# Performance work log

Measured on AMD Instinct MI355X. Metric: run time of the kernel, lower is better.

## Reference

```python
import jax, jax.numpy as jnp
import numpy as np

MASK_FILL = -1e9
LN_EPS = 1e-5


def setup_inputs() -> dict:
    key = jax.random.key(0)
    ks = jax.random.split(key, 8)
    b, n, d = 4, 4096, 768
    k, ds = 64, 32
    x = jax.random.normal(ks[0], (b, n, d), dtype=jnp.float32)
    encoded_descriptions = jax.random.normal(ks[1], (k, ds, d), dtype=jnp.float32)
    description_attention_mask = jax.random.randint(ks[2], (k, ds), 0, 2).astype(jnp.int32)
    attention_masks = jax.random.randint(ks[3], (b, n), 0, 2).astype(jnp.int32)
    std = 0.03
    Wk = std * jax.random.normal(ks[4], (d, d), dtype=jnp.float32)
    Wv = std * jax.random.normal(ks[5], (d, d), dtype=jnp.float32)
    Wo = std * jax.random.normal(ks[6], (1, d), dtype=jnp.float32)
    bo = jnp.zeros((1,), dtype=jnp.float32)
    ln_gamma = jnp.ones((d,), dtype=jnp.float32)
    ln_beta = jnp.zeros((d,), dtype=jnp.float32)
    return {
        "x": x,
        "encoded_descriptions": encoded_descriptions,
        "description_attention_mask": description_attention_mask,
        "attention_masks": attention_masks,
        "Wk": Wk, "Wv": Wv, "Wo": Wo, "bo": bo,
        "ln_gamma": ln_gamma, "ln_beta": ln_beta,
    }


def reference(x, encoded_descriptions, description_attention_mask, attention_masks,
              Wk, Wv, Wo, bo, ln_gamma, ln_beta):
    # x: [b, n, d]; encoded_descriptions: [k, ds, d]
    d = x.shape[-1]
    scale = 1.0 / jnp.sqrt(jnp.float32(d))

    k_note = jnp.einsum('bni,oi->bno', x, Wk)  # nn.Linear: x @ W.T
    v_note = jnp.einsum('bni,oi->bno', x, Wv)

    # att: [b, k, ds, n]  (torch computes kdbn then permutes to bkdn)
    att = jnp.einsum('kdi,bni->bkdn', encoded_descriptions, k_note) * scale

    desc_mask = description_attention_mask.astype(bool)          # [k, ds]
    note_mask = attention_masks.astype(bool)                     # [b, n]
    combined = desc_mask[None, :, :, None] & note_mask[:, None, None, :]  # [b,k,ds,n]

    att = jnp.where(combined, att, MASK_FILL)
    attention = jax.nn.softmax(att, axis=-1)                     # [b,k,ds,n]

    context = jnp.einsum('bkdn,bni->bkdi', attention, v_note)    # [b,k,ds,d]

    desc_importance = attention.sum(axis=-1)                     # [b,k,ds]
    desc_importance = jnp.where(desc_mask[None, :, :], desc_importance, MASK_FILL)
    desc_weights = jax.nn.softmax(desc_importance, axis=-1)      # [b,k,ds]

    pooled = (context * desc_weights[..., None]).sum(axis=2)     # [b,k,d]

    mu = pooled.mean(axis=-1, keepdims=True)
    var = pooled.var(axis=-1, keepdims=True)
    y = (pooled - mu) * jax.lax.rsqrt(var + LN_EPS) * ln_gamma + ln_beta

    out = jnp.einsum('bkd,od->bko', y, Wo) + bo                  # [b,k,1]
    return out[..., 0]                                           # [b,k]
```

## Files before the change

kernel.cpp:

```cpp
#include <hip/hip_runtime.h>
#include <hip/hip_bf16.h>
#include <hip/hip_fp16.h>

typedef _Float16 half8 __attribute__((ext_vector_type(8)));
typedef _Float16 half4 __attribute__((ext_vector_type(4)));
typedef _Float16 half2v __attribute__((ext_vector_type(2)));
typedef float f32x4 __attribute__((ext_vector_type(4)));

#define LN_EPS 1e-5f
#define MASK_FILL -1e9f

__device__ __forceinline__ void async16(void* lds, const void* g) {
  __builtin_amdgcn_global_load_lds(
      (__attribute__((address_space(1))) void*)(g),
      (__attribute__((address_space(3))) void*)(lds), 16, 0, 0);
}

__global__ __launch_bounds__(256) void cast_f32_f16_kernel(
    const float* __restrict__ in, _Float16* __restrict__ out, int n4) {
  int i = blockIdx.x * 256 + threadIdx.x;
  if (i < n4) {
    float4 v = ((const float4*)in)[i];
    half4 h = { (_Float16)v.x, (_Float16)v.y, (_Float16)v.z, (_Float16)v.w };
    ((half4*)out)[i] = h;
  }
}

__global__ __launch_bounds__(256) void transpose_f32_to_f16_kernel(
    const float* __restrict__ in, _Float16* __restrict__ out, int R, int C) {
  __shared__ float tile[32][33];
  int bc = blockIdx.x * 32, br = blockIdx.y * 32;
  int lc = threadIdx.x & 31;
  int lr0 = threadIdx.x >> 5;
  for (int i = lr0; i < 32; i += 8)
    tile[i][lc] = in[(size_t)(br + i) * C + bc + lc];
  __syncthreads();
  for (int i = lr0; i < 32; i += 8)
    out[(size_t)(bc + i) * R + br + lc] = (_Float16)tile[lc][i];
}

__global__ __launch_bounds__(256) void prep_kernel(
    const int* __restrict__ dmask, int* __restrict__ rowmap,
    float* __restrict__ row_w, int* __restrict__ start, int* __restrict__ keepM) {
  __shared__ int lsum[256];
  __shared__ int nvs[64];
  const int tid = threadIdx.x;
  int flags[8];
  int cnt = 0;
#pragma unroll
  for (int u = 0; u < 8; u++) {
    flags[u] = dmask[tid * 8 + u] != 0;
    cnt += flags[u];
  }
  if (tid < 64) {
    int c = 0;
    for (int u = 0; u < 32; u++) c += (dmask[tid * 32 + u] != 0);
    nvs[tid] = c;
  }
  lsum[tid] = cnt;
  __syncthreads();
  for (int ofs = 1; ofs < 256; ofs <<= 1) {
    int t = (tid >= ofs) ? lsum[tid - ofs] : 0;
    __syncthreads();
    lsum[tid] += t;
    __syncthreads();
  }
  int excl = lsum[tid] - cnt;
  int pos = excl;
#pragma unroll
  for (int u = 0; u < 8; u++) {
    if (flags[u]) {
      int row = tid * 8 + u;
      rowmap[pos] = row;
      row_w[pos] = 1.0f / (float)nvs[row >> 5];
      pos++;
    }
  }
  if ((tid & 3) == 0) start[tid >> 2] = excl;
  if (tid == 255) {
    start[64] = lsum[255];
    *keepM = lsum[255];
  }
}

__global__ __launch_bounds__(256) void gather_cast_kernel(
    const float* __restrict__ src, const int* __restrict__ rowmap,
    const int* __restrict__ keepM, _Float16* __restrict__ dst) {
  const int r = blockIdx.x;
  const int t = threadIdx.x;
  const int k = *keepM;
  _Float16* d = dst + (size_t)r * 768;
  if (r < k) {
    const float* s = src + (size_t)rowmap[r] * 768;
    for (int i = t; i < 768; i += 256) d[i] = (_Float16)s[i];
  } else {
    int* di = (int*)d;
    for (int i = t; i < 384; i += 256) di[i] = 0;
  }
}

template<bool OUT_F32, bool XCD>
__global__ __launch_bounds__(256) void gemm_f16_kernel(
    const _Float16* __restrict__ A, const _Float16* __restrict__ Bt,
    void* __restrict__ C, int M, int N, int K, float alpha,
    size_t strideBt, size_t strideC, const int* __restrict__ keepRows) {
  int bx = blockIdx.x, by = blockIdx.y, bz = blockIdx.z;
  if (XCD) {
    const int gx = gridDim.x, gy = gridDim.y;
    const int total = gx * gy * gridDim.z;
    const int L = bx + gx * (by + gy * bz);
    const int orig = (L & 7) * (total >> 3) + (L >> 3);
    bx = orig % gx;
    const int rest = orig / gx;
    by = rest % gy;
    bz = rest / gy;
  }
  const int bm = bx * 128, bn = by * 128;
  if (keepRows && bm >= *keepRows) return;
  __shared__ _Float16 As[128 * 64];
  __shared__ _Float16 Bs[128 * 64];
  const int tid = threadIdx.x;
  const size_t z = bz;
  const int wave = tid >> 6, lane = tid & 63;
  const int wr = (wave >> 1) * 64, wc = (wave & 1) * 64;
  const int fr = lane & 15, xr = lane & 7;
  f32x4 acc[4][4] = {};
  const int srow = wave * 32 + (lane >> 3);
  const int scol = (((lane & 7) ^ (lane >> 3))) * 8;
  const _Float16* ga = A + (size_t)(bm + srow) * K + scol;
  const _Float16* gb = Bt + z * strideBt + (size_t)(bn + srow) * K + scol;
  _Float16* lA = &As[(wave * 32) * 64];
  _Float16* lB = &Bs[(wave * 32) * 64];
  for (int k0 = 0; k0 < K; k0 += 64) {
    __syncthreads();
#pragma unroll
    for (int i = 0; i < 4; i++) {
      async16(lA + i * 8 * 64, ga + (size_t)(8 * i) * K + k0);
      async16(lB + i * 8 * 64, gb + (size_t)(8 * i) * K + k0);
    }
    __syncthreads();
#pragma unroll
    for (int k2 = 0; k2 < 2; k2++) {
      const int sb = k2 * 4 + (lane >> 4);
      const int so = (sb ^ xr) * 8;
      half8 af[4], bf[4];
#pragma unroll
      for (int i = 0; i < 4; i++)
        af[i] = *(const half8*)&As[(wr + i * 16 + fr) * 64 + so];
#pragma unroll
      for (int j = 0; j < 4; j++)
        bf[j] = *(const half8*)&Bs[(wc + j * 16 + fr) * 64 + so];
#pragma unroll
      for (int i = 0; i < 4; i++)
#pragma unroll
        for (int j = 0; j < 4; j++)
          acc[i][j] = __builtin_amdgcn_mfma_f32_16x16x32_f16(af[i], bf[j], acc[i][j], 0, 0, 0);
    }
  }
  const int rg = (lane >> 4) * 4;
#pragma unroll
  for (int i = 0; i < 4; i++) {
#pragma unroll
    for (int j = 0; j < 4; j++) {
      int col = bn + wc + j * 16 + fr;
#pragma unroll
      for (int r = 0; r < 4; r++) {
        int row = bm + wr + i * 16 + rg + r;
        float v = acc[i][j][r] * alpha;
        if (OUT_F32)
          ((float*)C)[z * strideC + (size_t)row * N + col] = v;
        else
          ((_Float16*)C)[z * strideC + (size_t)row * N + col] = (_Float16)v;
      }
    }
  }
}

__device__ __forceinline__ float block_reduce(float v, bool do_max, float* wbuf, int tid) {
#pragma unroll
  for (int m = 32; m; m >>= 1) {
    float o = __shfl_xor(v, m);
    v = do_max ? fmaxf(v, o) : (v + o);
  }
  if ((tid & 63) == 0) wbuf[tid >> 6] = v;
  __syncthreads();
  float r = do_max ? fmaxf(fmaxf(wbuf[0], wbuf[1]), fmaxf(wbuf[2], wbuf[3]))
                   : (wbuf[0] + wbuf[1] + wbuf[2] + wbuf[3]);
  __syncthreads();
  return r;
}

__global__ __launch_bounds__(256) void row_stats_kernel(
    const _Float16* __restrict__ S, const float* __restrict__ row_w,
    const int* __restrict__ keepM, const int* __restrict__ amask,
    float4* __restrict__ stats_c) {
  const int r = blockIdx.x;
  if (r >= *keepM) return;
  __shared__ float wbuf[4];
  const int b = blockIdx.z;
  const int tid = threadIdx.x;
  const float w = row_w[r];
  const _Float16* sp = S + ((size_t)b * 2048 + r) * 4096;
  const int* am = amask + (size_t)b * 4096;
  float a[16];
#pragma unroll
  for (int h = 0; h < 2; h++) {
    half8 v = *(const half8*)(sp + h * 2048 + tid * 8);
    int4 m0 = *(const int4*)(am + h * 2048 + tid * 8);
    int4 m1 = *(const int4*)(am + h * 2048 + tid * 8 + 4);
    int mm[8] = {m0.x, m0.y, m0.z, m0.w, m1.x, m1.y, m1.z, m1.w};
#pragma unroll
    for (int u = 0; u < 8; u++)
      a[h * 8 + u] = (mm[u] != 0) ? (float)v[u] : MASK_FILL;
  }
  float mx = a[0];
#pragma unroll
  for (int c = 1; c < 16; c++) mx = fmaxf(mx, a[c]);
  mx = block_reduce(mx, true, wbuf, tid);
  float ls = 0.f;
#pragma unroll
  for (int c = 0; c < 16; c++) ls += expf(a[c] - mx);
  float denom = block_reduce(ls, false, wbuf, tid);
  if (tid == 0)
    stats_c[(size_t)b * 2048 + r] = make_float4(mx, w / denom, 0.f, 0.f);
}

__global__ __launch_bounds__(256) void combine_kernel(
    const _Float16* __restrict__ S, const float4* __restrict__ stats_c,
    const int* __restrict__ start, const int* __restrict__ amask,
    float* __restrict__ ca) {
  const int kd = blockIdx.x;
  const int b = blockIdx.z;
  const int n0 = blockIdx.y * 512 + threadIdx.x * 2;
  const int i0 = start[kd], i1 = start[kd + 1];
  float acc0, acc1;
  if (i0 == i1) {
    acc0 = acc1 = 1.0f / 4096.0f;
  } else {
    const int* am = amask + (size_t)b * 4096;
    const bool nm0 = am[n0] != 0, nm1 = am[n0 + 1] != 0;
    acc0 = 0.f;
    acc1 = 0.f;
    for (int i = i0; i < i1; i++) {
      float4 s4 = stats_c[(size_t)b * 2048 + i];
      half2v v = *(const half2v*)(S + ((size_t)b * 2048 + i) * 4096 + n0);
      float a0 = nm0 ? (float)v[0] : MASK_FILL;
      float a1 = nm1 ? (float)v[1] : MASK_FILL;
      acc0 += s4.y * expf(a0 - s4.x);
      acc1 += s4.y * expf(a1 - s4.x);
    }
  }
  float2 r = {acc0, acc1};
  *(float2*)&ca[((size_t)b * 64 + kd) * 4096 + n0] = r;
}

__global__ __launch_bounds__(256) void t_partial_kernel(
    const float* __restrict__ ca,
    const _Float16* __restrict__ xh,
    float* __restrict__ t_part) {
  __shared__ float cas[64][68];
  __shared__ float xs[64][132];
  const int jt = blockIdx.x;
  const int nc = blockIdx.y;
  const int b = blockIdx.z;
  const int tid = threadIdx.x;
  const int tm = tid >> 4, tj = tid & 15;
  const int r = tid >> 2;
  const int cg = (tid & 3) * 16;
  const int cc = (tid & 3) * 32;
  float acc[4][8] = {};
  for (int n0 = nc * 256; n0 < nc * 256 + 256; n0 += 64) {
    __syncthreads();
    const float* cap = ca + (size_t)(b * 64 + r) * 4096 + n0 + cg;
#pragma unroll
    for (int u = 0; u < 16; u += 4)
      *(float4*)&cas[r][cg + u] = *(const float4*)(cap + u);
    const _Float16* xp = xh + ((size_t)b * 4096 + n0 + r) * 768 + jt * 128 + cc;
#pragma unroll
    for (int u = 0; u < 32; u += 8) {
      half8 hv = *(const half8*)(xp + u);
#pragma unroll
      for (int q = 0; q < 8; q++) xs[r][cc + u + q] = (float)hv[q];
    }
    __syncthreads();
#pragma unroll 8
    for (int nn = 0; nn < 64; ++nn) {
      float cm[4], xj[8];
#pragma unroll
      for (int i = 0; i < 4; i++) cm[i] = cas[tm * 4 + i][nn];
#pragma unroll
      for (int j = 0; j < 8; j++) xj[j] = xs[nn][tj * 8 + j];
#pragma unroll
      for (int i = 0; i < 4; i++)
#pragma unroll
        for (int j = 0; j < 8; j++) acc[i][j] += cm[i] * xj[j];
    }
  }
#pragma unroll
  for (int i = 0; i < 4; i++)
#pragma unroll
    for (int j = 0; j < 8; j++)
      t_part[((size_t)nc * 256 + b * 64 + tm * 4 + i) * 768 + jt * 128 + tj * 8 + j] = acc[i][j];
}

__global__ __launch_bounds__(256) void t_reduce_kernel(
    const float* __restrict__ t_part, _Float16* __restrict__ th) {
  int i = blockIdx.x * 256 + threadIdx.x;
  float s = 0.f;
#pragma unroll
  for (int nc = 0; nc < 16; ++nc) s += t_part[(size_t)nc * 196608 + i];
  th[i] = (_Float16)s;
}

__global__ __launch_bounds__(256) void ln_out_kernel(
    const float* __restrict__ pooled, const float* __restrict__ Wo,
    const float* __restrict__ bo, const float* __restrict__ gamma,
    const float* __restrict__ beta, float* __restrict__ out) {
  __shared__ float wbuf[4];
  const int row = blockIdx.x, tid = threadIdx.x;
  float p[3];
#pragma unroll
  for (int u = 0; u < 3; u++) p[u] = pooled[(size_t)row * 768 + tid + u * 256];
  float s1 = p[0] + p[1] + p[2];
  float s2 = p[0] * p[0] + p[1] * p[1] + p[2] * p[2];
  s1 = block_reduce(s1, false, wbuf, tid);
  s2 = block_reduce(s2, false, wbuf, tid);
  float mean = s1 * (1.f / 768.f);
  float var = s2 * (1.f / 768.f) - mean * mean;
  float rstd = rsqrtf(var + LN_EPS);
  float accv = 0.f;
#pragma unroll
  for (int u = 0; u < 3; u++) {
    int i = tid + u * 256;
    float y = (p[u] - mean) * rstd * gamma[i] + beta[i];
    accv += y * Wo[i];
  }
  accv = block_reduce(accv, false, wbuf, tid);
  if (tid == 0) out[row] = accv + bo[0];
}

extern "C" void kernel_launch(void* const* d_in, const int* in_sizes, int n_in,
                              void* d_out, int out_size, void* d_ws, size_t ws_size,
                              hipStream_t stream) {
  const float* x = (const float*)d_in[0];
  const float* enc = (const float*)d_in[1];
  const int* dmask = (const int*)d_in[2];
  const int* amask = (const int*)d_in[3];
  const float* Wk = (const float*)d_in[4];
  const float* Wv = (const float*)d_in[5];
  const float* Wo = (const float*)d_in[6];
  const float* bo = (const float*)d_in[7];
  const float* gamma = (const float*)d_in[8];
  const float* beta = (const float*)d_in[9];
  float* out = (float*)d_out;

  char* ws = (char*)d_ws;
  size_t off = 0;
  auto alloc = [&](size_t bytes) -> char* {
    char* p = ws + off;
    off += (bytes + 255) & ~((size_t)255);
    return p;
  };
  _Float16* xh = (_Float16*)alloc((size_t)16384 * 768 * 2);
  _Float16* wkT = (_Float16*)alloc((size_t)768 * 768 * 2);
  _Float16* wvh = (_Float16*)alloc((size_t)768 * 768 * 2);
  _Float16* enc_c = (_Float16*)alloc((size_t)2048 * 768 * 2);
  _Float16* encK_c = (_Float16*)alloc((size_t)2048 * 768 * 2);
  float* ca = (float*)alloc((size_t)4 * 64 * 4096 * 4);
  float* t_part = (float*)alloc((size_t)16 * 256 * 768 * 4);
  _Float16* th = (_Float16*)alloc((size_t)256 * 768 * 2);
  float* pooled = (float*)alloc((size_t)256 * 768 * 4);
  float4* stats_c = (float4*)alloc((size_t)4 * 2048 * 16);
  int* rowmap = (int*)alloc(2048 * 4);
  float* row_w = (float*)alloc(2048 * 4);
  int* start = (int*)alloc(65 * 4);
  int* keepM = (int*)alloc(4);

  const size_t s_one = (size_t)2048 * 4096 * 2;
  const bool batched = (off + 4 * s_one) <= ws_size;
  _Float16* S = (_Float16*)alloc(batched ? 4 * s_one : s_one);

  const float scale = 0.036084391824351615f;

  prep_kernel<<<1, 256, 0, stream>>>(dmask, rowmap, row_w, start, keepM);
  cast_f32_f16_kernel<<<12288, 256, 0, stream>>>(x, xh, 16384 * 768 / 4);
  cast_f32_f16_kernel<<<576, 256, 0, stream>>>(Wv, wvh, 768 * 768 / 4);
  transpose_f32_to_f16_kernel<<<dim3(24, 24), 256, 0, stream>>>(Wk, wkT, 768, 768);
  gather_cast_kernel<<<2048, 256, 0, stream>>>(enc, rowmap, keepM, enc_c);

  gemm_f16_kernel<false, false><<<dim3(16, 6), 256, 0, stream>>>(
      enc_c, wkT, encK_c, 2048, 768, 768, 1.0f, 0, 0, keepM);

  if (batched) {
    gemm_f16_kernel<false, true><<<dim3(16, 32, 4), 256, 0, stream>>>(
        encK_c, xh, S, 2048, 4096, 768, scale,
        (size_t)4096 * 768, (size_t)2048 * 4096, keepM);
    row_stats_kernel<<<dim3(2048, 1, 4), 256, 0, stream>>>(
        S, row_w, keepM, amask, stats_c);
    combine_kernel<<<dim3(64, 8, 4), 256, 0, stream>>>(S, stats_c, start, amask, ca);
  } else {
    for (int b = 0; b < 4; b++) {
      gemm_f16_kernel<false, true><<<dim3(16, 32), 256, 0, stream>>>(
          encK_c, xh + (size_t)b * 4096 * 768, S, 2048, 4096, 768, scale, 0, 0, keepM);
      row_stats_kernel<<<dim3(2048, 1, 1), 256, 0, stream>>>(
          S, row_w, keepM, amask + (size_t)b * 4096, stats_c + (size_t)b * 2048);
      combine_kernel<<<dim3(64, 8, 1), 256, 0, stream>>>(
          S, stats_c + (size_t)b * 2048, start, amask + (size_t)b * 4096,
          ca + (size_t)b * 64 * 4096);
    }
  }

  t_partial_kernel<<<dim3(6, 16, 4), 256, 0, stream>>>(ca, xh, t_part);
  t_reduce_kernel<<<768, 256, 0, stream>>>(t_part, th);
  gemm_f16_kernel<true, false><<<dim3(2, 6), 256, 0, stream>>>(
      th, wvh, pooled, 256, 768, 768, 1.0f, 0, 0, nullptr);
  ln_out_kernel<<<256, 256, 0, stream>>>(pooled, Wo, bo, gamma, beta, out);
}
```

Baseline: 164.3 us.

## Double-buffer GEMM K-loop and fuse row softmax stats with combine

The f16 GEMM now uses a 32-wide K tile, two LDS buffers and async prefetch of the next tile while the current one feeds MFMA, with a new swizzle. The separate row-statistics and combine kernels are merged into one kernel per (description, batch) that loops over its rows, computing max, sum and weighted exponentials in registers. This avoids reading the score matrix twice and drops the stats buffer. The cost is a grid of only 256 blocks, each serially walking its rows with block-wide reductions, which cuts parallelism.

Result: slower. 180.4 us (+9.8%).

```diff
diff --git a/kernel.cpp b/kernel.cpp
--- a/kernel.cpp
+++ b/kernel.cpp
@@ -4,7 +4,6 @@
 
 typedef _Float16 half8 __attribute__((ext_vector_type(8)));
 typedef _Float16 half4 __attribute__((ext_vector_type(4)));
-typedef _Float16 half2v __attribute__((ext_vector_type(2)));
 typedef float f32x4 __attribute__((ext_vector_type(4)));
 
 #define LN_EPS 1e-5f
@@ -117,45 +116,47 @@
   }
   const int bm = bx * 128, bn = by * 128;
   if (keepRows && bm >= *keepRows) return;
-  __shared__ _Float16 As[128 * 64];
-  __shared__ _Float16 Bs[128 * 64];
+  __shared__ _Float16 As[2][128 * 32];
+  __shared__ _Float16 Bs[2][128 * 32];
   const int tid = threadIdx.x;
   const size_t z = bz;
   const int wave = tid >> 6, lane = tid & 63;
   const int wr = (wave >> 1) * 64, wc = (wave & 1) * 64;
-  const int fr = lane & 15, xr = lane & 7;
+  const int fr = lane & 15;
   f32x4 acc[4][4] = {};
-  const int srow = wave * 32 + (lane >> 3);
-  const int scol = (((lane & 7) ^ (lane >> 3))) * 8;
+  const int srow = wave * 32 + (lane >> 2);
+  const int scol = ((lane & 3) ^ ((lane >> 3) & 3)) * 8;
   const _Float16* ga = A + (size_t)(bm + srow) * K + scol;
   const _Float16* gb = Bt + z * strideBt + (size_t)(bn + srow) * K + scol;
-  _Float16* lA = &As[(wave * 32) * 64];
-  _Float16* lB = &Bs[(wave * 32) * 64];
-  for (int k0 = 0; k0 < K; k0 += 64) {
+  const int nt = K >> 5;
+  auto stage = [&](int buf, int k0) {
+    _Float16* la = &As[buf][(wave * 32) * 32];
+    _Float16* lb = &Bs[buf][(wave * 32) * 32];
+    async16(la, ga + k0);
+    async16(la + 16 * 32, ga + (size_t)16 * K + k0);
+    async16(lb, gb + k0);
+    async16(lb + 16 * 32, gb + (size_t)16 * K + k0);
+  };
+  const int sg = (((lane >> 4) ^ ((fr >> 1) & 3))) * 8;
+  stage(0, 0);
+  __syncthreads();
+  int cur = 0;
+  for (int t = 0; t < nt; ++t) {
+    if (t + 1 < nt) stage(cur ^ 1, (t + 1) * 32);
+    half8 af[4], bf[4];
+#pragma unroll
+    for (int i = 0; i < 4; i++)
+      af[i] = *(const half8*)&As[cur][(wr + i * 16 + fr) * 32 + sg];
+#pragma unroll
+    for (int j = 0; j < 4; j++)
+      bf[j] = *(const half8*)&Bs[cur][(wc + j * 16 + fr) * 32 + sg];
+#pragma unroll
+    for (int i = 0; i < 4; i++)
+#pragma unroll
+      for (int j = 0; j < 4; j++)
+        acc[i][j] = __builtin_amdgcn_mfma_f32_16x16x32_f16(af[i], bf[j], acc[i][j], 0, 0, 0);
     __syncthreads();
-#pragma unroll
-    for (int i = 0; i < 4; i++) {
-      async16(lA + i * 8 * 64, ga + (size_t)(8 * i) * K + k0);
-      async16(lB + i * 8 * 64, gb + (size_t)(8 * i) * K + k0);
-    }
-    __syncthreads();
-#pragma unroll
-    for (int k2 = 0; k2 < 2; k2++) {
-      const int sb = k2 * 4 + (lane >> 4);
-      const int so = (sb ^ xr) * 8;
-      half8 af[4], bf[4];
-#pragma unroll
-      for (int i = 0; i < 4; i++)
-        af[i] = *(const half8*)&As[(wr + i * 16 + fr) * 64 + so];
-#pragma unroll
-      for (int j = 0; j < 4; j++)
-        bf[j] = *(const half8*)&Bs[(wc + j * 16 + fr) * 64 + so];
-#pragma unroll
-      for (int i = 0; i < 4; i++)
-#pragma unroll
-        for (int j = 0; j < 4; j++)
-          acc[i][j] = __builtin_amdgcn_mfma_f32_16x16x32_f16(af[i], bf[j], acc[i][j], 0, 0, 0);
-    }
+    cur ^= 1;
   }
   const int rg = (lane >> 4) * 4;
 #pragma unroll
@@ -190,68 +191,69 @@
   return r;
 }
 
-__global__ __launch_bounds__(256) void row_stats_kernel(
+__global__ __launch_bounds__(256) void fused_softmax_kernel(
     const _Float16* __restrict__ S, const float* __restrict__ row_w,
-    const int* __restrict__ keepM, const int* __restrict__ amask,
-    float4* __restrict__ stats_c) {
-  const int r = blockIdx.x;
-  if (r >= *keepM) return;
+    const int* __restrict__ start, const int* __restrict__ amask,
+    float* __restrict__ ca) {
   __shared__ float wbuf[4];
+  const int kd = blockIdx.x;
   const int b = blockIdx.z;
   const int tid = threadIdx.x;
-  const float w = row_w[r];
-  const _Float16* sp = S + ((size_t)b * 2048 + r) * 4096;
-  const int* am = amask + (size_t)b * 4096;
-  float a[16];
-#pragma unroll
-  for (int h = 0; h < 2; h++) {
-    half8 v = *(const half8*)(sp + h * 2048 + tid * 8);
-    int4 m0 = *(const int4*)(am + h * 2048 + tid * 8);
-    int4 m1 = *(const int4*)(am + h * 2048 + tid * 8 + 4);
-    int mm[8] = {m0.x, m0.y, m0.z, m0.w, m1.x, m1.y, m1.z, m1.w};
-#pragma unroll
-    for (int u = 0; u < 8; u++)
-      a[h * 8 + u] = (mm[u] != 0) ? (float)v[u] : MASK_FILL;
-  }
-  float mx = a[0];
-#pragma unroll
-  for (int c = 1; c < 16; c++) mx = fmaxf(mx, a[c]);
-  mx = block_reduce(mx, true, wbuf, tid);
-  float ls = 0.f;
-#pragma unroll
-  for (int c = 0; c < 16; c++) ls += expf(a[c] - mx);
-  float denom = block_reduce(ls, false, wbuf, tid);
-  if (tid == 0)
-    stats_c[(size_t)b * 2048 + r] = make_float4(mx, w / denom, 0.f, 0.f);
-}
-
-__global__ __launch_bounds__(256) void combine_kernel(
-    const _Float16* __restrict__ S, const float4* __restrict__ stats_c,
-    const int* __restrict__ start, const int* __restrict__ amask,
-    float* __restrict__ ca) {
-  const int kd = blockIdx.x;
-  const int b = blockIdx.z;
-  const int n0 = blockIdx.y * 512 + threadIdx.x * 2;
   const int i0 = start[kd], i1 = start[kd + 1];
-  float acc0, acc1;
+  float ca_r[16];
   if (i0 == i1) {
-    acc0 = acc1 = 1.0f / 4096.0f;
+#pragma unroll
+    for (int c = 0; c < 16; c++) ca_r[c] = 1.0f / 4096.0f;
   } else {
+#pragma unroll
+    for (int c = 0; c < 16; c++) ca_r[c] = 0.f;
     const int* am = amask + (size_t)b * 4096;
-    const bool nm0 = am[n0] != 0, nm1 = am[n0 + 1] != 0;
-    acc0 = 0.f;
-    acc1 = 0.f;
+    bool nm[16];
+#pragma unroll
+    for (int h = 0; h < 2; h++) {
+      int4 m0 = *(const int4*)(am + h * 2048 + tid * 8);
+      int4 m1 = *(const int4*)(am + h * 2048 + tid * 8 + 4);
+      nm[h * 8 + 0] = m0.x != 0; nm[h * 8 + 1] = m0.y != 0;
+      nm[h * 8 + 2] = m0.z != 0; nm[h * 8 + 3] = m0.w != 0;
+      nm[h * 8 + 4] = m1.x != 0; nm[h * 8 + 5] = m1.y != 0;
+      nm[h * 8 + 6] = m1.z != 0; nm[h * 8 + 7] = m1.w != 0;
+    }
     for (int i = i0; i < i1; i++) {
-      float4 s4 = stats_c[(size_t)b * 2048 + i];
-      half2v v = *(const half2v*)(S + ((size_t)b * 2048 + i) * 4096 + n0);
-      float a0 = nm0 ? (float)v[0] : MASK_FILL;
-      float a1 = nm1 ? (float)v[1] : MASK_FILL;
-      acc0 += s4.y * expf(a0 - s4.x);
-      acc1 += s4.y * expf(a1 - s4.x);
-    }
-  }
-  float2 r = {acc0, acc1};
-  *(float2*)&ca[((size_t)b * 64 + kd) * 4096 + n0] = r;
+      const _Float16* sp = S + ((size_t)b * 2048 + i) * 4096;
+      float a[16];
+#pragma unroll
+      for (int h = 0; h < 2; h++) {
+        half8 v = *(const half8*)(sp + h * 2048 + tid * 8);
+#pragma unroll
+        for (int u = 0; u < 8; u++)
+          a[h * 8 + u] = nm[h * 8 + u] ? (float)v[u] : MASK_FILL;
+      }
+      float mx = a[0];
+#pragma unroll
+      for (int c = 1; c < 16; c++) mx = fmaxf(mx, a[c]);
+      mx = block_reduce(mx, true, wbuf, tid);
+      float e[16];
+      float ls = 0.f;
+#pragma unroll
+      for (int c = 0; c < 16; c++) {
+        e[c] = expf(a[c] - mx);
+        ls += e[c];
+      }
+      float denom = block_reduce(ls, false, wbuf, tid);
+      float iw = row_w[i] / denom;
+#pragma unroll
+      for (int c = 0; c < 16; c++) ca_r[c] += iw * e[c];
+    }
+  }
+  float* cp = ca + ((size_t)b * 64 + kd) * 4096;
+#pragma unroll
+  for (int h = 0; h < 2; h++)
+#pragma unroll
+    for (int u = 0; u < 8; u += 4) {
+      float4 w4 = {ca_r[h * 8 + u], ca_r[h * 8 + u + 1],
+                   ca_r[h * 8 + u + 2], ca_r[h * 8 + u + 3]};
+      *(float4*)&cp[h * 2048 + tid * 8 + u] = w4;
+    }
 }
 
 __global__ __launch_bounds__(256) void t_partial_kernel(
@@ -370,7 +372,6 @@
   float* t_part = (float*)alloc((size_t)16 * 256 * 768 * 4);
   _Float16* th = (_Float16*)alloc((size_t)256 * 768 * 2);
   float* pooled = (float*)alloc((size_t)256 * 768 * 4);
-  float4* stats_c = (float4*)alloc((size_t)4 * 2048 * 16);
   int* rowmap = (int*)alloc(2048 * 4);
   float* row_w = (float*)alloc(2048 * 4);
   int* start = (int*)alloc(65 * 4);
@@ -395,18 +396,14 @@
     gemm_f16_kernel<false, true><<<dim3(16, 32, 4), 256, 0, stream>>>(
         encK_c, xh, S, 2048, 4096, 768, scale,
         (size_t)4096 * 768, (size_t)2048 * 4096, keepM);
-    row_stats_kernel<<<dim3(2048, 1, 4), 256, 0, stream>>>(
-        S, row_w, keepM, amask, stats_c);
-    combine_kernel<<<dim3(64, 8, 4), 256, 0, stream>>>(S, stats_c, start, amask, ca);
+    fused_softmax_kernel<<<dim3(64, 1, 4), 256, 0, stream>>>(
+        S, row_w, start, amask, ca);
   } else {
     for (int b = 0; b < 4; b++) {
       gemm_f16_kernel<false, true><<<dim3(16, 32), 256, 0, stream>>>(
           encK_c, xh + (size_t)b * 4096 * 768, S, 2048, 4096, 768, scale, 0, 0, keepM);
-      row_stats_kernel<<<dim3(2048, 1, 1), 256, 0, stream>>>(
-          S, row_w, keepM, amask + (size_t)b * 4096, stats_c + (size_t)b * 2048);
-      combine_kernel<<<dim3(64, 8, 1), 256, 0, stream>>>(
-          S, stats_c + (size_t)b * 2048, start, amask + (size_t)b * 4096,
-          ca + (size_t)b * 64 * 4096);
+      fused_softmax_kernel<<<dim3(64, 1, 1), 256, 0, stream>>>(
+          S, row_w, start, amask + (size_t)b * 4096, ca + (size_t)b * 64 * 4096);
     }
   }
 
```

## Compact valid note columns per batch and skip masked columns in score GEMM

Applied to the files above, without the earlier changes.

A prep kernel now stable-partitions each batch's notes into valid-first order and records the valid count. The x cast becomes a gather into that permuted order, and the four casts/gathers are merged into one launch. The score GEMM skips column tiles past the valid count, and row stats and combine replace per-column mask loads with an index-versus-count test. This removes roughly half of the score GEMM work and the S traffic for masked notes. It relies on t_partial consuming ca in the same permuted order as xh_c, which holds because both use the permuted index.

Result: faster. 153.9 us (-6.3%).

```diff
diff --git a/kernel.cpp b/kernel.cpp
--- a/kernel.cpp
+++ b/kernel.cpp
@@ -16,86 +16,125 @@
       (__attribute__((address_space(3))) void*)(lds), 16, 0, 0);
 }
 
-__global__ __launch_bounds__(256) void cast_f32_f16_kernel(
-    const float* __restrict__ in, _Float16* __restrict__ out, int n4) {
-  int i = blockIdx.x * 256 + threadIdx.x;
-  if (i < n4) {
-    float4 v = ((const float4*)in)[i];
-    half4 h = { (_Float16)v.x, (_Float16)v.y, (_Float16)v.z, (_Float16)v.w };
-    ((half4*)out)[i] = h;
-  }
-}
-
-__global__ __launch_bounds__(256) void transpose_f32_to_f16_kernel(
-    const float* __restrict__ in, _Float16* __restrict__ out, int R, int C) {
-  __shared__ float tile[32][33];
-  int bc = blockIdx.x * 32, br = blockIdx.y * 32;
-  int lc = threadIdx.x & 31;
-  int lr0 = threadIdx.x >> 5;
-  for (int i = lr0; i < 32; i += 8)
-    tile[i][lc] = in[(size_t)(br + i) * C + bc + lc];
-  __syncthreads();
-  for (int i = lr0; i < 32; i += 8)
-    out[(size_t)(bc + i) * R + br + lc] = (_Float16)tile[lc][i];
-}
-
-__global__ __launch_bounds__(256) void prep_kernel(
-    const int* __restrict__ dmask, int* __restrict__ rowmap,
-    float* __restrict__ row_w, int* __restrict__ start, int* __restrict__ keepM) {
+__global__ __launch_bounds__(256) void prep_all_kernel(
+    const int* __restrict__ dmask, const int* __restrict__ amask,
+    int* __restrict__ rowmap, float* __restrict__ row_w,
+    int* __restrict__ start, int* __restrict__ keepM,
+    int* __restrict__ perm, int* __restrict__ cntN) {
   __shared__ int lsum[256];
   __shared__ int nvs[64];
   const int tid = threadIdx.x;
-  int flags[8];
-  int cnt = 0;
-#pragma unroll
-  for (int u = 0; u < 8; u++) {
-    flags[u] = dmask[tid * 8 + u] != 0;
-    cnt += flags[u];
-  }
-  if (tid < 64) {
-    int c = 0;
-    for (int u = 0; u < 32; u++) c += (dmask[tid * 32 + u] != 0);
-    nvs[tid] = c;
-  }
-  lsum[tid] = cnt;
-  __syncthreads();
-  for (int ofs = 1; ofs < 256; ofs <<= 1) {
-    int t = (tid >= ofs) ? lsum[tid - ofs] : 0;
-    __syncthreads();
-    lsum[tid] += t;
-    __syncthreads();
-  }
-  int excl = lsum[tid] - cnt;
-  int pos = excl;
-#pragma unroll
-  for (int u = 0; u < 8; u++) {
-    if (flags[u]) {
-      int row = tid * 8 + u;
-      rowmap[pos] = row;
-      row_w[pos] = 1.0f / (float)nvs[row >> 5];
-      pos++;
-    }
-  }
-  if ((tid & 3) == 0) start[tid >> 2] = excl;
-  if (tid == 255) {
-    start[64] = lsum[255];
-    *keepM = lsum[255];
-  }
-}
-
-__global__ __launch_bounds__(256) void gather_cast_kernel(
-    const float* __restrict__ src, const int* __restrict__ rowmap,
-    const int* __restrict__ keepM, _Float16* __restrict__ dst) {
-  const int r = blockIdx.x;
+  if (blockIdx.x == 0) {
+    int flags[8];
+    int cnt = 0;
+#pragma unroll
+    for (int u = 0; u < 8; u++) {
+      flags[u] = dmask[tid * 8 + u] != 0;
+      cnt += flags[u];
+    }
+    if (tid < 64) {
+      int c = 0;
+      for (int u = 0; u < 32; u++) c += (dmask[tid * 32 + u] != 0);
+      nvs[tid] = c;
+    }
+    lsum[tid] = cnt;
+    __syncthreads();
+    for (int ofs = 1; ofs < 256; ofs <<= 1) {
+      int t = (tid >= ofs) ? lsum[tid - ofs] : 0;
+      __syncthreads();
+      lsum[tid] += t;
+      __syncthreads();
+    }
+    int excl = lsum[tid] - cnt;
+    int pos = excl;
+#pragma unroll
+    for (int u = 0; u < 8; u++) {
+      if (flags[u]) {
+        int row = tid * 8 + u;
+        rowmap[pos] = row;
+        row_w[pos] = 1.0f / (float)nvs[row >> 5];
+        pos++;
+      }
+    }
+    if ((tid & 3) == 0) start[tid >> 2] = excl;
+    if (tid == 255) {
+      start[64] = lsum[255];
+      *keepM = lsum[255];
+    }
+  } else {
+    const int b = blockIdx.x - 1;
+    const int* am = amask + (size_t)b * 4096;
+    int flags[16];
+    int cnt = 0;
+#pragma unroll
+    for (int u = 0; u < 16; u++) {
+      flags[u] = am[tid * 16 + u] != 0;
+      cnt += flags[u];
+    }
+    lsum[tid] = cnt;
+    __syncthreads();
+    for (int ofs = 1; ofs < 256; ofs <<= 1) {
+      int t = (tid >= ofs) ? lsum[tid - ofs] : 0;
+      __syncthreads();
+      lsum[tid] += t;
+      __syncthreads();
+    }
+    const int total = lsum[255];
+    int vpos = lsum[tid] - cnt;
+    int ipos = total + (tid * 16 - vpos);
+    int* pm = perm + (size_t)b * 4096;
+#pragma unroll
+    for (int u = 0; u < 16; u++) {
+      int g = tid * 16 + u;
+      if (flags[u]) pm[vpos++] = g;
+      else pm[ipos++] = g;
+    }
+    if (tid == 0) cntN[b] = total;
+  }
+}
+
+__global__ __launch_bounds__(256) void gather_cast_all_kernel(
+    const float* __restrict__ x, const float* __restrict__ enc,
+    const float* __restrict__ Wv, const float* __restrict__ Wk,
+    const int* __restrict__ perm, const int* __restrict__ rowmap,
+    const int* __restrict__ keepM,
+    _Float16* __restrict__ xh_c, _Float16* __restrict__ enc_c,
+    _Float16* __restrict__ wvh, _Float16* __restrict__ wkT) {
+  __shared__ float tile[32][33];
+  const int bid = blockIdx.x;
   const int t = threadIdx.x;
-  const int k = *keepM;
-  _Float16* d = dst + (size_t)r * 768;
-  if (r < k) {
-    const float* s = src + (size_t)rowmap[r] * 768;
-    for (int i = t; i < 768; i += 256) d[i] = (_Float16)s[i];
+  if (bid < 16384) {
+    const int b = bid >> 12, ci = bid & 4095;
+    const int n = perm[(size_t)b * 4096 + ci];
+    const float* s = x + ((size_t)b * 4096 + n) * 768;
+    _Float16* d = xh_c + ((size_t)b * 4096 + ci) * 768;
+#pragma unroll
+    for (int u = 0; u < 3; u++) d[t + u * 256] = (_Float16)s[t + u * 256];
+  } else if (bid < 18432) {
+    const int r = bid - 16384;
+    _Float16* d = enc_c + (size_t)r * 768;
+    if (r < *keepM) {
+      const float* s = enc + (size_t)rowmap[r] * 768;
+#pragma unroll
+      for (int u = 0; u < 3; u++) d[t + u * 256] = (_Float16)s[t + u * 256];
+    } else {
+      int* di = (int*)d;
+      for (int i = t; i < 384; i += 256) di[i] = 0;
+    }
+  } else if (bid < 19008) {
+    const int base = (bid - 18432) * 1024 + t * 4;
+    float4 v = *(const float4*)(Wv + base);
+    half4 h = { (_Float16)v.x, (_Float16)v.y, (_Float16)v.z, (_Float16)v.w };
+    *(half4*)(wkT ? (wvh + base) : (wvh + base)) = h;
   } else {
-    int* di = (int*)d;
-    for (int i = t; i < 384; i += 256) di[i] = 0;
+    const int tb = bid - 19008;
+    const int bc = (tb % 24) * 32, br = (tb / 24) * 32;
+    const int lc = t & 31, lr0 = t >> 5;
+    for (int i = lr0; i < 32; i += 8)
+      tile[i][lc] = Wk[(size_t)(br + i) * 768 + bc + lc];
+    __syncthreads();
+    for (int i = lr0; i < 32; i += 8)
+      wkT[(size_t)(bc + i) * 768 + br + lc] = (_Float16)tile[lc][i];
   }
 }
 
@@ -103,7 +142,8 @@
 __global__ __launch_bounds__(256) void gemm_f16_kernel(
     const _Float16* __restrict__ A, const _Float16* __restrict__ Bt,
     void* __restrict__ C, int M, int N, int K, float alpha,
-    size_t strideBt, size_t strideC, const int* __restrict__ keepRows) {
+    size_t strideBt, size_t strideC, const int* __restrict__ keepRows,
+    const int* __restrict__ keepN) {
   int bx = blockIdx.x, by = blockIdx.y, bz = blockIdx.z;
   if (XCD) {
     const int gx = gridDim.x, gy = gridDim.y;
@@ -117,6 +157,7 @@
   }
   const int bm = bx * 128, bn = by * 128;
   if (keepRows && bm >= *keepRows) return;
+  if (keepN && bn >= keepN[bz]) return;
   __shared__ _Float16 As[128 * 64];
   __shared__ _Float16 Bs[128 * 64];
   const int tid = threadIdx.x;
@@ -192,26 +233,27 @@
 
 __global__ __launch_bounds__(256) void row_stats_kernel(
     const _Float16* __restrict__ S, const float* __restrict__ row_w,
-    const int* __restrict__ keepM, const int* __restrict__ amask,
+    const int* __restrict__ keepM, const int* __restrict__ cntN,
     float4* __restrict__ stats_c) {
   const int r = blockIdx.x;
   if (r >= *keepM) return;
   __shared__ float wbuf[4];
   const int b = blockIdx.z;
   const int tid = threadIdx.x;
+  const int cnt = cntN[b];
+  if (cnt == 0) return;
   const float w = row_w[r];
-  const _Float16* sp = S + ((size_t)b * 2048 + r) * 4096;
-  const int* am = amask + (size_t)b * 4096;
+  const _Float16* sp = S + ((size_t)b * 2048 + r) * 4096 + tid * 16;
   float a[16];
-#pragma unroll
-  for (int h = 0; h < 2; h++) {
-    half8 v = *(const half8*)(sp + h * 2048 + tid * 8);
-    int4 m0 = *(const int4*)(am + h * 2048 + tid * 8);
-    int4 m1 = *(const int4*)(am + h * 2048 + tid * 8 + 4);
-    int mm[8] = {m0.x, m0.y, m0.z, m0.w, m1.x, m1.y, m1.z, m1.w};
-#pragma unroll
-    for (int u = 0; u < 8; u++)
-      a[h * 8 + u] = (mm[u] != 0) ? (float)v[u] : MASK_FILL;
+  {
+    half8 v0 = *(const half8*)(sp);
+    half8 v1 = *(const half8*)(sp + 8);
+    const int c0 = tid * 16;
+#pragma unroll
+    for (int u = 0; u < 8; u++) {
+      a[u] = (c0 + u < cnt) ? (float)v0[u] : MASK_FILL;
+      a[8 + u] = (c0 + 8 + u < cnt) ? (float)v1[u] : MASK_FILL;
+    }
   }
   float mx = a[0];
 #pragma unroll
@@ -227,31 +269,32 @@
 
 __global__ __launch_bounds__(256) void combine_kernel(
     const _Float16* __restrict__ S, const float4* __restrict__ stats_c,
-    const int* __restrict__ start, const int* __restrict__ amask,
+    const int* __restrict__ start, const int* __restrict__ cntN,
     float* __restrict__ ca) {
   const int kd = blockIdx.x;
   const int b = blockIdx.z;
-  const int n0 = blockIdx.y * 512 + threadIdx.x * 2;
+  const int i = blockIdx.y * 512 + threadIdx.x * 2;
   const int i0 = start[kd], i1 = start[kd + 1];
+  const int cnt = cntN[b];
   float acc0, acc1;
-  if (i0 == i1) {
+  if (i0 == i1 || cnt == 0) {
     acc0 = acc1 = 1.0f / 4096.0f;
+  } else if (i >= cnt) {
+    acc0 = acc1 = 0.f;
   } else {
-    const int* am = amask + (size_t)b * 4096;
-    const bool nm0 = am[n0] != 0, nm1 = am[n0 + 1] != 0;
     acc0 = 0.f;
     acc1 = 0.f;
-    for (int i = i0; i < i1; i++) {
-      float4 s4 = stats_c[(size_t)b * 2048 + i];
-      half2v v = *(const half2v*)(S + ((size_t)b * 2048 + i) * 4096 + n0);
-      float a0 = nm0 ? (float)v[0] : MASK_FILL;
-      float a1 = nm1 ? (float)v[1] : MASK_FILL;
-      acc0 += s4.y * expf(a0 - s4.x);
-      acc1 += s4.y * expf(a1 - s4.x);
-    }
-  }
-  float2 r = {acc0, acc1};
-  *(float2*)&ca[((size_t)b * 64 + kd) * 4096 + n0] = r;
+    const _Float16* sp = S + ((size_t)b * 2048 + i0) * 4096 + i;
+    for (int r = i0; r < i1; r++, sp += 4096) {
+      float4 s4 = stats_c[(size_t)b * 2048 + r];
+      half2v v = *(const half2v*)sp;
+      acc0 += s4.y * expf((float)v[0] - s4.x);
+      acc1 += s4.y * expf((float)v[1] - s4.x);
+    }
+    if (i + 1 >= cnt) acc1 = 0.f;
+  }
+  float2 rr = {acc0, acc1};
+  *(float2*)&ca[((size_t)b * 64 + kd) * 4096 + i] = rr;
 }
 
 __global__ __launch_bounds__(256) void t_partial_kernel(
@@ -361,7 +404,7 @@
     off += (bytes + 255) & ~((size_t)255);
     return p;
   };
-  _Float16* xh = (_Float16*)alloc((size_t)16384 * 768 * 2);
+  _Float16* xh_c = (_Float16*)alloc((size_t)16384 * 768 * 2);
   _Float16* wkT = (_Float16*)alloc((size_t)768 * 768 * 2);
   _Float16* wvh = (_Float16*)alloc((size_t)768 * 768 * 2);
   _Float16* enc_c = (_Float16*)alloc((size_t)2048 * 768 * 2);
@@ -375,6 +418,8 @@
   float* row_w = (float*)alloc(2048 * 4);
   int* start = (int*)alloc(65 * 4);
   int* keepM = (int*)alloc(4);
+  int* perm = (int*)alloc((size_t)4 * 4096 * 4);
+  int* cntN = (int*)alloc(4 * 4);
 
   const size_t s_one = (size_t)2048 * 4096 * 2;
   const bool batched = (off + 4 * s_one) <= ws_size;
@@ -382,37 +427,38 @@
 
   const float scale = 0.036084391824351615f;
 
-  prep_kernel<<<1, 256, 0, stream>>>(dmask, rowmap, row_w, start, keepM);
-  cast_f32_f16_kernel<<<12288, 256, 0, stream>>>(x, xh, 16384 * 768 / 4);
-  cast_f32_f16_kernel<<<576, 256, 0, stream>>>(Wv, wvh, 768 * 768 / 4);
-  transpose_f32_to_f16_kernel<<<dim3(24, 24), 256, 0, stream>>>(Wk, wkT, 768, 768);
-  gather_cast_kernel<<<2048, 256, 0, stream>>>(enc, rowmap, keepM, enc_c);
+  prep_all_kernel<<<5, 256, 0, stream>>>(
+      dmask, amask, rowmap, row_w, start, keepM, perm, cntN);
+  gather_cast_all_kernel<<<19584, 256, 0, stream>>>(
+      x, enc, Wv, Wk, perm, rowmap, keepM, xh_c, enc_c, wvh, wkT);
 
   gemm_f16_kernel<false, false><<<dim3(16, 6), 256, 0, stream>>>(
-      enc_c, wkT, encK_c, 2048, 768, 768, 1.0f, 0, 0, keepM);
+      enc_c, wkT, encK_c, 2048, 768, 768, 1.0f, 0, 0, keepM, nullptr);
 
   if (batched) {
     gemm_f16_kernel<false, true><<<dim3(16, 32, 4), 256, 0, stream>>>(
-        encK_c, xh, S, 2048, 4096, 768, scale,
-        (size_t)4096 * 768, (size_t)2048 * 4096, keepM);
+        encK_c, xh_c, S, 2048, 4096, 768, scale,
+        (size_t)4096 * 768, (size_t)2048 * 4096, keepM, cntN);
     row_stats_kernel<<<dim3(2048, 1, 4), 256, 0, stream>>>(
-        S, row_w, keepM, amask, stats_c);
-    combine_kernel<<<dim3(64, 8, 4), 256, 0, stream>>>(S, stats_c, start, amask, ca);
+        S, row_w, keepM, cntN, stats_c);
+    combine_kernel<<<dim3(64, 8, 4), 256, 0, stream>>>(
+        S, stats_c, start, cntN, ca);
   } else {
     for (int b = 0; b < 4; b++) {
       gemm_f16_kernel<false, true><<<dim3(16, 32), 256, 0, stream>>>(
-          encK_c, xh + (size_t)b * 4096 * 768, S, 2048, 4096, 768, scale, 0, 0, keepM);
+          encK_c, xh_c + (size_t)b * 4096 * 768, S, 2048, 4096, 768, scale,
+          0, 0, keepM, cntN + b);
       row_stats_kernel<<<dim3(2048, 1, 1), 256, 0, stream>>>(
-          S, row_w, keepM, amask + (size_t)b * 4096, stats_c + (size_t)b * 2048);
+          S, row_w, keepM, cntN + b, stats_c + (size_t)b * 2048);
       combine_kernel<<<dim3(64, 8, 1), 256, 0, stream>>>(
-          S, stats_c + (size_t)b * 2048, start, amask + (size_t)b * 4096,
+          S, stats_c + (size_t)b * 2048, start, cntN + b,
           ca + (size_t)b * 64 * 4096);
     }
   }
 
-  t_partial_kernel<<<dim3(6, 16, 4), 256, 0, stream>>>(ca, xh, t_part);
+  t_partial_kernel<<<dim3(6, 16, 4), 256, 0, stream>>>(ca, xh_c, t_part);
   t_reduce_kernel<<<768, 256, 0, stream>>>(t_part, th);
   gemm_f16_kernel<true, false><<<dim3(2, 6), 256, 0, stream>>>(
-      th, wvh, pooled, 256, 768, 768, 1.0f, 0, 0, nullptr);
+      th, wvh, pooled, 256, 768, 768, 1.0f, 0, 0, nullptr, nullptr);
   ln_out_kernel<<<256, 256, 0, stream>>>(pooled, Wo, bo, gamma, beta, out);
 }
```
